# Kernel optimization log

Hardware: AMD Instinct MI355X
Metric: run time of the kernel (lower is better)

Reference implementation:

```python
import jax, jax.numpy as jnp
import numpy as np

EPS = 1e-9
TOP_K = 2
CAPACITY_FACTOR = 4.0
MIN_EXPERT_CAPACITY = 4


def setup_inputs() -> dict:
    key = jax.random.key(0)
    k1, k2 = jax.random.split(key)
    x = jax.random.normal(k1, (4, 32, 512, 24, 24), dtype=jnp.float32)
    w_gating = jax.random.normal(k2, (512, 16), dtype=jnp.float32)
    return {"x": x, "w_gating": w_gating}


def cumsum_exclusive(t, axis):
    # exclusive cumsum along `axis`: cumsum shifted by one (zero first)
    return jnp.cumsum(t, axis=axis) - t


def reference(x, w_gating):
    T, B, D, H, W = x.shape
    N = H * W                       # group_size (tokens per image)
    E = w_gating.shape[1]           # num_gates / experts
    dt = x.dtype

    # pool over timesteps: (T,B,D,H,W) -> (B,N,D)
    x_tok = x.reshape(T, B, D, N).transpose(0, 1, 3, 2)
    x_pooled = x_tok.mean(axis=0)

    raw_gates = jax.nn.softmax(jnp.einsum('bnd,de->bne', x_pooled, w_gating), axis=-1)

    # --- top-k selection loop (importance=None, so no importance masking) ---
    gates_remaining = raw_gates
    masks, gates, indices = [], [], []
    for k in range(TOP_K):
        index_k = jnp.argmax(gates_remaining, axis=-1)                 # (B,N)
        gate_k = jnp.take_along_axis(gates_remaining, index_k[..., None], axis=-1)[..., 0]
        mask_k = jax.nn.one_hot(index_k, E, dtype=dt)                  # (B,N,E)
        masks.append(mask_k)
        gates.append(gate_k)
        indices.append(index_k)
        gates_remaining = gates_remaining * (1.0 - mask_k)

    gate_sum = sum(gates) + EPS
    gates = [g / gate_sum for g in gates]

    # load-balancing loss
    density_1 = masks[0].mean(axis=-2)          # (B,E)
    density_1_proxy = raw_gates.mean(axis=-2)   # (B,E)
    loss = (density_1_proxy * density_1).mean() * float(E ** 2)

    # policy == 'all': masks unchanged

    expert_capacity = min(N, int(N * CAPACITY_FACTOR / E))
    expert_capacity = max(expert_capacity, MIN_EXPERT_CAPACITY)
    cap_f = float(expert_capacity)

    # --- capacity assignment ---
    cumulative_position = jnp.zeros((B, 1, E), dtype=dt)
    positions = [None] * TOP_K
    for k in range(TOP_K):
        position_k = cumsum_exclusive(masks[k], axis=-2) + cumulative_position
        position_k = position_k * masks[k]
        masks[k] = masks[k] * (position_k < cap_f).astype(dt)
        positions[k] = position_k.sum(axis=-1)                          # (B,N)
        gates[k] = gates[k] * masks[k].sum(axis=-1)
        cumulative_position = cumulative_position + masks[k].sum(axis=-2, keepdims=True)

    # --- combine / dispatch tensors (B, N, E, C) ---
    combine_tensor = jnp.zeros((B, N, E, expert_capacity), dtype=dt)
    for k in range(TOP_K):
        mask_k_flat = masks[k].sum(axis=-1)                             # (B,N)
        expert_oh = jax.nn.one_hot(indices[k], E, dtype=dt)             # (B,N,E)
        # out-of-range positions produce all-zero rows, matching safe_one_hot's slice
        pos_oh = jax.nn.one_hot(positions[k].astype(jnp.int32), expert_capacity, dtype=dt)  # (B,N,C)
        combine_tensor = combine_tensor + (
            (gates[k] * mask_k_flat)[..., None, None]
            * expert_oh[..., None]
            * pos_oh[..., None, :]
        )
    dispatch_tensor = (combine_tensor != 0).astype(dt)
    return dispatch_tensor, combine_tensor, loss
```

## Files before the change

### kernel.cpp

```cpp
#include <hip/hip_runtime.h>

#define TT 4
#define BB 32
#define DD 512
#define NN 576
#define EE 16
#define DC 8
#define DCH 64
#define CC 144
#define ROW (EE*CC)
#define SZ 42467328UL

typedef float f4 __attribute__((ext_vector_type(4)));

__global__ __launch_bounds__(256) void k_zero(float* __restrict__ out) {
  const size_t total = 2 * SZ / 4;
  f4* o = (f4*)out;
  const f4 zv = {0.f, 0.f, 0.f, 0.f};
  for (size_t idx = (size_t)blockIdx.x * 256 + threadIdx.x; idx < total;
       idx += (size_t)2048 * 256)
    __builtin_nontemporal_store(zv, &o[idx]);
}

__global__ __launch_bounds__(576) void k_part(const float* __restrict__ x,
                                              const float* __restrict__ w,
                                              float* __restrict__ part) {
  const int b  = blockIdx.x;
  const int dc = blockIdx.y;
  const int n  = threadIdx.x;
  const int d0 = dc * DCH;

  const float* xp = x + ((size_t)b * DD + d0) * NN + n;
  const size_t TS = (size_t)BB * DD * NN;

  float acc[EE];
#pragma unroll
  for (int e = 0; e < EE; ++e) acc[e] = 0.f;

#pragma unroll 4
  for (int dd = 0; dd < DCH; ++dd) {
    const size_t o = (size_t)dd * NN;
    const float x0 = xp[o];
    const float x1 = xp[o + TS];
    const float x2 = xp[o + 2 * TS];
    const float x3 = xp[o + 3 * TS];
    const float xs = (x0 + x1) + (x2 + x3);
    const float* wd = w + (size_t)(d0 + dd) * EE;
#pragma unroll
    for (int e = 0; e < EE; ++e) acc[e] = fmaf(xs, wd[e], acc[e]);
  }

  float4* dst4 = (float4*)(part + (((size_t)b * NN + n) * DC + dc) * EE);
#pragma unroll
  for (int q = 0; q < 4; ++q)
    dst4[q] = make_float4(acc[4*q], acc[4*q+1], acc[4*q+2], acc[4*q+3]);
}

__global__ __launch_bounds__(576) void k_gate(const float* __restrict__ part,
                                              float4* __restrict__ info,
                                              float* __restrict__ lossp) {
  const int b = blockIdx.x;
  const int n = threadIdx.x;
  const int wave = n >> 6, lane = n & 63;

  __shared__ float sprox[9][EE];
  __shared__ int   swc1[9][EE];
  __shared__ int   swc2[9][EE];
  __shared__ int   woff1[9][EE];
  __shared__ int   woff2[9][EE];
  __shared__ float sproxTot[EE];
  __shared__ int   scnt0[EE];
  __shared__ int   sbase2[EE];

  float l[EE];
#pragma unroll
  for (int e = 0; e < EE; ++e) l[e] = 0.f;
  {
    const float4* p4 = (const float4*)(part + (size_t)(b * NN + n) * (DC * EE));
#pragma unroll
    for (int dc = 0; dc < DC; ++dc) {
#pragma unroll
      for (int q = 0; q < 4; ++q) {
        float4 v = p4[dc * 4 + q];
        l[4*q+0] += v.x; l[4*q+1] += v.y; l[4*q+2] += v.z; l[4*q+3] += v.w;
      }
    }
#pragma unroll
    for (int e = 0; e < EE; ++e) l[e] *= 0.25f;
  }

  float m = l[0];
#pragma unroll
  for (int e = 1; e < EE; ++e) m = fmaxf(m, l[e]);
  float raw[EE]; float s = 0.f;
#pragma unroll
  for (int e = 0; e < EE; ++e) { raw[e] = expf(l[e] - m); s += raw[e]; }
  float inv = 1.f / s;
#pragma unroll
  for (int e = 0; e < EE; ++e) raw[e] *= inv;

  int e1 = 0; float g1 = raw[0];
#pragma unroll
  for (int e = 1; e < EE; ++e) if (raw[e] > g1) { g1 = raw[e]; e1 = e; }
  int e2 = (e1 == 0) ? 1 : 0; float g2 = raw[e2];
#pragma unroll
  for (int e = 0; e < EE; ++e) if (e != e1 && raw[e] > g2) { g2 = raw[e]; e2 = e; }
  const float denom = g1 + g2 + 1e-9f;
  const float w0 = g1 / denom, w1 = g2 / denom;

  const unsigned long long ltm = (1ull << lane) - 1ull;
  int pre1 = 0, pre2 = 0;
#pragma unroll
  for (int e = 0; e < EE; ++e) {
    unsigned long long m1 = __ballot(e1 == e);
    unsigned long long m2 = __ballot(e2 == e);
    if (lane == 0) { swc1[wave][e] = __popcll(m1); swc2[wave][e] = __popcll(m2); }
    if (e == e1) pre1 = __popcll(m1 & ltm);
    if (e == e2) pre2 = __popcll(m2 & ltm);
  }

#pragma unroll
  for (int e = 0; e < EE; ++e) {
    float v = raw[e];
#pragma unroll
    for (int off = 32; off; off >>= 1) v += __shfl_xor(v, off);
    if (lane == 0) sprox[wave][e] = v;
  }
  __syncthreads();

  if (n < EE) {
    int r1 = 0, r2 = 0; float pv = 0.f;
#pragma unroll
    for (int wv = 0; wv < 9; ++wv) {
      woff1[wv][n] = r1; r1 += swc1[wv][n];
      woff2[wv][n] = r2; r2 += swc2[wv][n];
      pv += sprox[wv][n];
    }
    scnt0[n]    = r1;
    sbase2[n]   = r1 < CC ? r1 : CC;
    sproxTot[n] = pv;
  }
  __syncthreads();

  if (n == 0) {
    float S = 0.f;
    for (int e = 0; e < EE; ++e) S += sproxTot[e] * (float)scnt0[e];
    lossp[b] = S / ((float)NN * (float)NN);
  }

  const int p0 = woff1[wave][e1] + pre1;
  const int p1 = sbase2[e2] + woff2[wave][e2] + pre2;

  const int  pos0 = (p0 < CC) ? (e1 * CC + p0) : -1;
  const int  pos1 = (p1 < CC) ? (e2 * CC + p1) : -1;
  const float w0k = (p0 < CC) ? w0 : 0.f;
  const float w1k = (p1 < CC) ? w1 : 0.f;

  float4 o;
  o.x = __int_as_float(pos0);
  o.y = w0k;
  o.z = __int_as_float(pos1);
  o.w = w1k;
  info[b * NN + n] = o;
}

__global__ __launch_bounds__(512) void k_scatter(const float4* __restrict__ info,
                                                 const float* __restrict__ lossp,
                                                 float* __restrict__ out) {
  const int tok = blockIdx.x * 512 + threadIdx.x;
  if (tok == 0) {
    float sv = 0.f;
    for (int b = 0; b < BB; ++b) sv += lossp[b];
    out[2 * SZ] = 0.5f * sv;
  }
  const float4 inf = info[tok];
  const int   pos0 = __float_as_int(inf.x);
  const int   pos1 = __float_as_int(inf.z);

  float* disp = out + (size_t)tok * ROW;
  float* comb = out + SZ + (size_t)tok * ROW;
  if (pos0 >= 0) { disp[pos0] = 1.f; comb[pos0] = inf.y; }
  if (pos1 >= 0) { disp[pos1] = 1.f; comb[pos1] = inf.w; }
}

extern "C" void kernel_launch(void* const* d_in, const int* in_sizes, int n_in,
                              void* d_out, int out_size, void* d_ws, size_t ws_size,
                              hipStream_t stream) {
  const float* x = (const float*)d_in[0];
  const float* w = (const float*)d_in[1];
  float* out = (float*)d_out;

  float*  part  = (float*)d_ws;
  float4* info  = (float4*)((char*)d_ws + 9437184);
  float*  lossp = (float*)((char*)d_ws + 9437184 + 294912);

  hipLaunchKernelGGL(k_zero,    dim3(2048), dim3(256), 0, stream, out);
  hipLaunchKernelGGL(k_part,    dim3(BB, DC), dim3(576), 0, stream, x, w, part);
  hipLaunchKernelGGL(k_gate,    dim3(BB),   dim3(576), 0, stream, part, info, lossp);
  hipLaunchKernelGGL(k_scatter, dim3(36),   dim3(512), 0, stream, info, lossp, out);
}
```

Baseline: 127.8 us.

## Fuse output zeroing and scatter into a single dense write kernel

Removes the separate zero-fill kernel and the sparse scatter kernel. A single grid-stride kernel now writes every float4 of the dispatch and combine tensors, computing each value from the per-token routing info. This avoids a second pass of scattered writes after the zero fill and saves one launch. In exchange, each store now needs an integer divide and a load of the token info, and the stores are regular rather than nontemporal.

```diff
diff --git a/kernel.cpp b/kernel.cpp
--- a/kernel.cpp
+++ b/kernel.cpp
@@ -10,17 +10,9 @@
 #define CC 144
 #define ROW (EE*CC)
 #define SZ 42467328UL
+#define T4 (SZ/4)
 
 typedef float f4 __attribute__((ext_vector_type(4)));
-
-__global__ __launch_bounds__(256) void k_zero(float* __restrict__ out) {
-  const size_t total = 2 * SZ / 4;
-  f4* o = (f4*)out;
-  const f4 zv = {0.f, 0.f, 0.f, 0.f};
-  for (size_t idx = (size_t)blockIdx.x * 256 + threadIdx.x; idx < total;
-       idx += (size_t)2048 * 256)
-    __builtin_nontemporal_store(zv, &o[idx]);
-}
 
 __global__ __launch_bounds__(576) void k_part(const float* __restrict__ x,
                                               const float* __restrict__ w,
@@ -164,23 +156,41 @@
   info[b * NN + n] = o;
 }
 
-__global__ __launch_bounds__(512) void k_scatter(const float4* __restrict__ info,
-                                                 const float* __restrict__ lossp,
-                                                 float* __restrict__ out) {
-  const int tok = blockIdx.x * 512 + threadIdx.x;
-  if (tok == 0) {
+__global__ __launch_bounds__(256) void k_write(const float4* __restrict__ info,
+                                               const float* __restrict__ lossp,
+                                               float* __restrict__ out) {
+  if (blockIdx.x == 0 && threadIdx.x == 0) {
     float sv = 0.f;
     for (int b = 0; b < BB; ++b) sv += lossp[b];
     out[2 * SZ] = 0.5f * sv;
   }
-  const float4 inf = info[tok];
-  const int   pos0 = __float_as_int(inf.x);
-  const int   pos1 = __float_as_int(inf.z);
-
-  float* disp = out + (size_t)tok * ROW;
-  float* comb = out + SZ + (size_t)tok * ROW;
-  if (pos0 >= 0) { disp[pos0] = 1.f; comb[pos0] = inf.y; }
-  if (pos1 >= 0) { disp[pos1] = 1.f; comb[pos1] = inf.w; }
+
+  f4* o = (f4*)out;
+  for (size_t idx = (size_t)blockIdx.x * 256 + threadIdx.x; idx < 2 * T4;
+       idx += (size_t)2048 * 256) {
+    const bool comb = idx >= T4;
+    const unsigned r = (unsigned)(comb ? idx - T4 : idx);
+    const unsigned tok = r / 576u;
+    const int f0 = (int)(r - tok * 576u) * 4;
+
+    const float4 inf = info[tok];
+    const int   pos0 = __float_as_int(inf.x);
+    const int   pos1 = __float_as_int(inf.z);
+
+    f4 v;
+    if (comb) {
+      v = f4{ (f0+0 == pos0) ? inf.y : ((f0+0 == pos1) ? inf.w : 0.f),
+              (f0+1 == pos0) ? inf.y : ((f0+1 == pos1) ? inf.w : 0.f),
+              (f0+2 == pos0) ? inf.y : ((f0+2 == pos1) ? inf.w : 0.f),
+              (f0+3 == pos0) ? inf.y : ((f0+3 == pos1) ? inf.w : 0.f) };
+    } else {
+      v = f4{ (f0+0 == pos0 || f0+0 == pos1) ? 1.f : 0.f,
+              (f0+1 == pos0 || f0+1 == pos1) ? 1.f : 0.f,
+              (f0+2 == pos0 || f0+2 == pos1) ? 1.f : 0.f,
+              (f0+3 == pos0 || f0+3 == pos1) ? 1.f : 0.f };
+    }
+    o[idx] = v;
+  }
 }
 
 extern "C" void kernel_launch(void* const* d_in, const int* in_sizes, int n_in,
@@ -194,8 +204,7 @@
   float4* info  = (float4*)((char*)d_ws + 9437184);
   float*  lossp = (float*)((char*)d_ws + 9437184 + 294912);
 
-  hipLaunchKernelGGL(k_zero,    dim3(2048), dim3(256), 0, stream, out);
-  hipLaunchKernelGGL(k_part,    dim3(BB, DC), dim3(576), 0, stream, x, w, part);
-  hipLaunchKernelGGL(k_gate,    dim3(BB),   dim3(576), 0, stream, part, info, lossp);
-  hipLaunchKernelGGL(k_scatter, dim3(36),   dim3(512), 0, stream, info, lossp, out);
-}
+  hipLaunchKernelGGL(k_part,  dim3(BB, DC), dim3(576), 0, stream, x, w, part);
+  hipLaunchKernelGGL(k_gate,  dim3(BB),     dim3(576), 0, stream, part, info, lossp);
+  hipLaunchKernelGGL(k_write, dim3(2048),   dim3(256), 0, stream, info, lossp, out);
+}
```

After: 125.1 us. -2.2%, faster.
